# Kernel optimization log

Measured on AMD Instinct MI355X. Metric: run time of the kernel, lower is better.

The kernel has to match this reference:

```python
import jax, jax.numpy as jnp
import numpy as np
from math import factorial

# (mul, l, parity) in mul_ir layout order
IRREPS_IN1 = [(128, 0, 1), (128, 1, -1), (128, 2, 1)]
IRREPS_IN2 = [(1, 0, 1), (1, 1, -1), (1, 2, 1)]
IRREPS_OUT = [(128, 0, 1), (128, 1, -1), (128, 2, 1)]
BATCH = 65536


def _f(n):
    return float(factorial(int(round(n))))


def _su2_cg(j1, j2, j3, m1, m2, m3):
    # <j1 m1 j2 m2 | j3 m3> (Racah formula, complex SU(2) basis)
    if m3 != m1 + m2:
        return 0.0
    vmin = int(max(-j1 + j2 + m3, -j1 + m1, 0))
    vmax = int(min(j2 + j3 + m1, j3 - j1 + j2, j3 + m3))
    C = ((2 * j3 + 1) * _f(j3 + j1 - j2) * _f(j3 - j1 + j2) * _f(j1 + j2 - j3)
         * _f(j3 + m3) * _f(j3 - m3)
         / (_f(j1 + j2 + j3 + 1) * _f(j1 - m1) * _f(j1 + m1) * _f(j2 - m2) * _f(j2 + m2))) ** 0.5
    S = 0.0
    for v in range(vmin, vmax + 1):
        S += (-1.0) ** (v + j2 + m2) * _f(j2 + j3 + m1 - v) * _f(j1 - m1 + v) / (
            _f(v) * _f(j3 - j1 + j2 - v) * _f(j3 + m3 - v) * _f(v + j1 - j2 - m3))
    return C * S


def _q(l):
    # change of basis real -> complex spherical harmonics (e3nn convention)
    q = np.zeros((2 * l + 1, 2 * l + 1), dtype=np.complex128)
    for m in range(-l, 0):
        q[l + m, l + abs(m)] = 1 / np.sqrt(2)
        q[l + m, l - abs(m)] = -1j / np.sqrt(2)
    q[l, l] = 1.0
    for m in range(1, l + 1):
        q[l + m, l + abs(m)] = (-1) ** m / np.sqrt(2)
        q[l + m, l - abs(m)] = 1j * (-1) ** m / np.sqrt(2)
    return (-1j) ** l * q


def _wigner_3j(l1, l2, l3):
    C = np.zeros((2 * l1 + 1, 2 * l2 + 1, 2 * l3 + 1))
    for m1 in range(-l1, l1 + 1):
        for m2 in range(-l2, l2 + 1):
            for m3 in range(-l3, l3 + 1):
                C[l1 + m1, l2 + m2, l3 + m3] = _su2_cg(l1, l2, l3, m1, m2, m3)
    Q1, Q2, Q3 = _q(l1), _q(l2), _q(l3)
    R = np.einsum('ij,kl,nm,ikn->jlm', Q1, Q2, np.conj(Q3), C.astype(np.complex128))
    return np.real(R) / np.sqrt(2 * l3 + 1)  # sum of squares == 1 (3j normalization)


def _slices(irreps):
    out, off = [], 0
    for mul, l, _ in irreps:
        out.append((off, mul, 2 * l + 1))
        off += mul * (2 * l + 1)
    return out, off


S1, DIM1 = _slices(IRREPS_IN1)
S2, DIM2 = _slices(IRREPS_IN2)
S3, DIM3 = _slices(IRREPS_OUT)

# fully-connected instruction list: all parity/triangle-allowed (i1, i2, i3) paths
_instr = [(i1, i2, i3)
          for i1, (_, l1, p1) in enumerate(IRREPS_IN1)
          for i2, (_, l2, p2) in enumerate(IRREPS_IN2)
          for i3, (_, l3, p3) in enumerate(IRREPS_OUT)
          if p1 * p2 == p3 and abs(l1 - l2) <= l3 <= l1 + l2]

# path normalization 'element': fan-in per output irrep = sum of mul1*mul2 over incoming paths
_fan = {}
for i1, i2, i3 in _instr:
    _fan[i3] = _fan.get(i3, 0) + IRREPS_IN1[i1][0] * IRREPS_IN2[i2][0]

PATHS, _off = [], 0
for i1, i2, i3 in _instr:
    mu1, l1, _ = IRREPS_IN1[i1]
    mu2, l2, _ = IRREPS_IN2[i2]
    mu3, l3, _ = IRREPS_OUT[i3]
    # irrep_normalization 'component' + path 'element': path_weight = sqrt((2l3+1)/fan)
    cg = _wigner_3j(l1, l2, l3) * np.sqrt((2 * l3 + 1) / _fan[i3])
    PATHS.append((i1, i2, i3, _off, (mu1, mu2, mu3), jnp.asarray(cg, dtype=jnp.float32)))
    _off += mu1 * mu2 * mu3
WEIGHT_NUMEL = _off  # 180224 for these irreps (11 paths x 128*1*128)


def _fctp(x1, x2, weight):
    w = weight.reshape(-1).astype(x1.dtype)
    acc = [None] * len(IRREPS_OUT)
    for i1, i2, i3, off, wshape, cg in PATHS:
        o1, mu1, d1 = S1[i1]
        o2, mu2, d2 = S2[i2]
        a = x1[:, o1:o1 + mu1 * d1].reshape(-1, mu1, d1)  # [B, u, i]
        b = x2[:, o2:o2 + mu2 * d2].reshape(-1, mu2, d2)  # [B, v, j]
        wp = w[off:off + wshape[0] * wshape[1] * wshape[2]].reshape(wshape)  # [u, v, w]
        c = jnp.einsum('bui,bvj,uvw,ijk->bwk', a, b, wp, cg.astype(x1.dtype))
        acc[i3] = c if acc[i3] is None else acc[i3] + c
    # mul_ir layout: flatten each (B, mul, 2l+1) segment and concatenate
    return jnp.concatenate([s.reshape(s.shape[0], -1) for s in acc], axis=-1)


def setup_inputs():
    key = jax.random.key(0)
    k1, k2, k3 = jax.random.split(key, 3)
    return {
        "x1": jax.random.normal(k1, (BATCH, DIM1), dtype=jnp.float32),
        "x2": jax.random.normal(k2, (BATCH, DIM2), dtype=jnp.float32),
        "weight": jax.random.normal(k3, (1, WEIGHT_NUMEL), dtype=jnp.float32),
    }


def reference(x1, x2, weight):
    return _fctp(x1, x2, weight)
```

## Files before the change

### kernel.cpp

```cpp
#include <hip/hip_runtime.h>
#include <hip/hip_bf16.h>

typedef __attribute__((ext_vector_type(8))) short bf16x8;
typedef __attribute__((ext_vector_type(4))) float f32x4;
typedef __attribute__((ext_vector_type(4))) unsigned int u32x4;
typedef __attribute__((ext_vector_type(4))) unsigned short u16x4;

__device__ __forceinline__ unsigned short f2bf(float f) {
  __hip_bfloat16 h = __float2bfloat16(f);
  return __builtin_bit_cast(unsigned short, h);
}
__device__ __forceinline__ float bfw(unsigned int word, int hi) {
  union { unsigned int i; float f; } v;
  v.i = hi ? (word & 0xffff0000u) : (word << 16);
  return v.f;
}

struct cplx { double re, im; };
__device__ __forceinline__ cplx cmul(cplx a, cplx b) {
  return {a.re * b.re - a.im * b.im, a.re * b.im + a.im * b.re};
}
__device__ __forceinline__ double fct_(int n) {
  const double f[8] = {1., 1., 2., 6., 24., 120., 720., 5040.};
  return f[n];
}
__device__ __forceinline__ int imax_(int a, int b) { return a > b ? a : b; }
__device__ __forceinline__ int imin_(int a, int b) { return a < b ? a : b; }

__device__ double su2_cg(int j1, int j2, int j3, int m1, int m2, int m3) {
  if (m3 != m1 + m2) return 0.0;
  int vmin = imax_(imax_(-j1 + j2 + m3, -j1 + m1), 0);
  int vmax = imin_(imin_(j2 + j3 + m1, j3 - j1 + j2), j3 + m3);
  double C = sqrt((2.0 * j3 + 1.0) * fct_(j3 + j1 - j2) * fct_(j3 - j1 + j2) * fct_(j1 + j2 - j3)
                  * fct_(j3 + m3) * fct_(j3 - m3)
                  / (fct_(j1 + j2 + j3 + 1) * fct_(j1 - m1) * fct_(j1 + m1) * fct_(j2 - m2) * fct_(j2 + m2)));
  double S = 0.0;
  for (int v = vmin; v <= vmax; ++v) {
    double sgn = ((v + j2 + m2) & 1) ? -1.0 : 1.0;
    S += sgn * fct_(j2 + j3 + m1 - v) * fct_(j1 - m1 + v)
         / (fct_(v) * fct_(j3 - j1 + j2 - v) * fct_(j3 + m3 - v) * fct_(v + j1 - j2 - m3));
  }
  return C * S;
}

__device__ cplx q_entry(int l, int r, int c) {
  const double s2 = 0.70710678118654752440;
  int m = r - l;
  cplx v = {0.0, 0.0};
  if (m < 0) {
    if (c == l - m) v = {s2, 0.0};
    else if (c == l + m) v = {0.0, -s2};
  } else if (m == 0) {
    if (c == l) v = {1.0, 0.0};
  } else {
    double sgn = (m & 1) ? -1.0 : 1.0;
    if (c == l + m) v = {sgn * s2, 0.0};
    else if (c == l - m) v = {0.0, sgn * s2};
  }
  cplx f;
  switch (l & 3) {
    case 0: f = {1.0, 0.0}; break;
    case 1: f = {0.0, -1.0}; break;
    case 2: f = {-1.0, 0.0}; break;
    default: f = {0.0, 1.0}; break;
  }
  return cmul(f, v);
}

__global__ void init_kernel(const float* __restrict__ w, unsigned short* __restrict__ Wt,
                            float* __restrict__ cgw) {
  const int blk = blockIdx.x;
  const int tid = threadIdx.x;
  if (blk < 704) {
    int g = blk * 256 + tid;
    int p = g >> 14, rem = g & 16383;
    int u = rem >> 7, wc = rem & 127;
    Wt[(p << 14) + (wc << 7) + u] = f2bf(w[g]);
    return;
  }
  const int p = blk - 704;
  const int L1t[11] = {0,0,0,1,1,1,1,2,2,2,2};
  const int L2t[11] = {0,1,2,0,1,1,2,0,1,2,2};
  const int L3t[11] = {0,1,2,1,0,2,1,2,1,0,2};
  const double FAN[11] = {384.,512.,512.,512.,384.,512.,512.,512.,512.,384.,512.};
  const int l1 = L1t[p], l2 = L2t[p], l3 = L3t[p];
  const int n1 = 2 * l1 + 1, n2 = 2 * l2 + 1, n3 = 2 * l3 + 1;
  if (tid >= n1 * n2 * n3) return;
  const int a = tid / (n2 * n3), b = (tid / n3) % n2, c = tid % n3;
  double sre = 0.0;
  for (int i = 0; i < n1; ++i)
    for (int k = 0; k < n2; ++k)
      for (int n = 0; n < n3; ++n) {
        double cg = su2_cg(l1, l2, l3, i - l1, k - l2, n - l3);
        if (cg == 0.0) continue;
        cplx q1 = q_entry(l1, i, a);
        cplx q2 = q_entry(l2, k, b);
        cplx q3 = q_entry(l3, n, c);
        q3.im = -q3.im;
        cplx pr = cmul(cmul(q1, q2), q3);
        sre += pr.re * cg;
      }
  cgw[p * 125 + a * 25 + b * 5 + c] = (float)(sre / sqrt(FAN[p]));
}

__device__ __forceinline__ void stage_all(const float* __restrict__ x1, int Mbase,
                                          unsigned short* __restrict__ s_a) {
  const int tid = threadIdx.x;
#pragma unroll 6
  for (int rep = 0; rep < 18; ++rep) {
    int it = tid + rep * 256;
    int row = it / 288, c4 = it % 288;
    int col = c4 << 2;
    const f32x4 v = __builtin_nontemporal_load(
        (const f32x4*)&x1[(size_t)(Mbase + row) * 1152 + col]);
    u16x4 h;
    h.x = f2bf(v.x); h.y = f2bf(v.y); h.z = f2bf(v.z); h.w = f2bf(v.w);
    int dst;
    if (col < 128)      dst = row * 136 + col;
    else if (col < 512) dst = 2176 + row * 392 + (col - 128);
    else                dst = 8448 + row * 648 + (col - 512);
    *(u16x4*)&s_a[dst] = h;
  }
}

template<int PID, int L1, int L2, int L3>
__device__ __forceinline__ void do_path(const float* __restrict__ cgw,
                                        const unsigned short* __restrict__ s_a,
                                        const unsigned short* __restrict__ Wt,
                                        const float (&x2v)[9],
                                        int kg, int r16, int nbase,
                                        f32x4 (&acc)[2 * L3 + 1][2]) {
  constexpr int D1 = 2 * L1 + 1, D2 = 2 * L2 + 1, D3 = 2 * L3 + 1;
  constexpr int O2 = (L2 == 0) ? 0 : ((L2 == 1) ? 1 : 4);
  constexpr int GB = (L1 == 0) ? 0 : ((L1 == 1) ? 2176 : 8448);
  constexpr int pitch = 128 * D1 + 8;
  float g[D1][D3];
#pragma unroll
  for (int i = 0; i < D1; ++i)
#pragma unroll
    for (int k = 0; k < D3; ++k) {
      float s = 0.f;
#pragma unroll
      for (int j = 0; j < D2; ++j)
        s += x2v[O2 + j] * cgw[PID * 125 + i * 25 + j * 5 + k];
      g[i][k] = s;
    }
  const unsigned short* __restrict__ wbase = Wt + (PID << 14);
  const unsigned short* __restrict__ ap0 = s_a + GB + r16 * pitch;
#pragma unroll 1
  for (int us = 0; us < 4; ++us) {
    const int u0 = us * 32 + kg * 8;
    const unsigned short* ap = ap0 + u0 * D1;
    u32x4 av[D1];
#pragma unroll
    for (int d = 0; d < D1; ++d) av[d] = *(const u32x4*)(ap + d * 8);
    u32x4 bw[2];
#pragma unroll
    for (int nf = 0; nf < 2; ++nf)
      bw[nf] = *(const u32x4*)&wbase[(nbase + nf * 16 + r16) * 128 + u0];
    unsigned int taw[D3][4];
#pragma unroll
    for (int jp = 0; jp < 4; ++jp) {
      float a0[D1], a1[D1];
#pragma unroll
      for (int i = 0; i < D1; ++i) {
        int e0 = (2 * jp) * D1 + i, e1 = e0 + D1;
        a0[i] = bfw(av[e0 >> 3][(e0 & 7) >> 1], e0 & 1);
        a1[i] = bfw(av[e1 >> 3][(e1 & 7) >> 1], e1 & 1);
      }
#pragma unroll
      for (int k = 0; k < D3; ++k) {
        float t0 = 0.f, t1 = 0.f;
#pragma unroll
        for (int i = 0; i < D1; ++i) { t0 += a0[i] * g[i][k]; t1 += a1[i] * g[i][k]; }
        taw[k][jp] = (unsigned int)f2bf(t0) | ((unsigned int)f2bf(t1) << 16);
      }
    }
#pragma unroll
    for (int k = 0; k < D3; ++k) {
      u32x4 tw;
      tw.x = taw[k][0]; tw.y = taw[k][1]; tw.z = taw[k][2]; tw.w = taw[k][3];
      bf16x8 ta = __builtin_bit_cast(bf16x8, tw);
#pragma unroll
      for (int nf = 0; nf < 2; ++nf)
        acc[k][nf] = __builtin_amdgcn_mfma_f32_16x16x32_bf16(
            ta, __builtin_bit_cast(bf16x8, bw[nf]), acc[k][nf], 0, 0, 0);
    }
  }
}

__global__ void __launch_bounds__(256, 2) fctp_main(
    const float* __restrict__ x1, const float* __restrict__ x2,
    const float* __restrict__ cgw, const unsigned short* __restrict__ Wt,
    float* __restrict__ out) {
  __shared__ __align__(16) unsigned short s_a[18816];
  const int tid = threadIdx.x;
  const int Mbase = blockIdx.x << 4;

  stage_all(x1, Mbase, s_a);

  const int lane = tid & 63, ni = tid >> 6;
  const int r16 = lane & 15, kg = lane >> 4;
  const int nbase = ni << 5;

  float x2v[9];
  const float* __restrict__ x2p = x2 + (size_t)(Mbase + r16) * 9;
#pragma unroll
  for (int j = 0; j < 9; ++j) x2v[j] = x2p[j];

  __syncthreads();

  const int bout = Mbase + (kg << 2);

  {
    f32x4 acc[1][2] = {};
    do_path<0, 0, 0, 0>(cgw, s_a, Wt, x2v, kg, r16, nbase, acc);
    do_path<4, 1, 1, 0>(cgw, s_a, Wt, x2v, kg, r16, nbase, acc);
    do_path<9, 2, 2, 0>(cgw, s_a, Wt, x2v, kg, r16, nbase, acc);
#pragma unroll
    for (int nf = 0; nf < 2; ++nf) {
      const int w = nbase + nf * 16 + r16;
#pragma unroll
      for (int r = 0; r < 4; ++r)
        __builtin_nontemporal_store(acc[0][nf][r],
                                    &out[(size_t)(bout + r) * 1152 + w]);
    }
  }
  {
    f32x4 acc[3][2] = {};
    do_path<1, 0, 1, 1>(cgw, s_a, Wt, x2v, kg, r16, nbase, acc);
    do_path<3, 1, 0, 1>(cgw, s_a, Wt, x2v, kg, r16, nbase, acc);
    do_path<6, 1, 2, 1>(cgw, s_a, Wt, x2v, kg, r16, nbase, acc);
    do_path<8, 2, 1, 1>(cgw, s_a, Wt, x2v, kg, r16, nbase, acc);
#pragma unroll
    for (int nf = 0; nf < 2; ++nf) {
      const int w = nbase + nf * 16 + r16;
#pragma unroll
      for (int r = 0; r < 4; ++r) {
        float* o = out + (size_t)(bout + r) * 1152 + 128 + w * 3;
#pragma unroll
        for (int k = 0; k < 3; ++k) o[k] = acc[k][nf][r];
      }
    }
  }
  {
    f32x4 acc[5][2] = {};
    do_path<2, 0, 2, 2>(cgw, s_a, Wt, x2v, kg, r16, nbase, acc);
    do_path<5, 1, 1, 2>(cgw, s_a, Wt, x2v, kg, r16, nbase, acc);
    do_path<7, 2, 0, 2>(cgw, s_a, Wt, x2v, kg, r16, nbase, acc);
    do_path<10, 2, 2, 2>(cgw, s_a, Wt, x2v, kg, r16, nbase, acc);
#pragma unroll
    for (int nf = 0; nf < 2; ++nf) {
      const int w = nbase + nf * 16 + r16;
#pragma unroll
      for (int r = 0; r < 4; ++r) {
        float* o = out + (size_t)(bout + r) * 1152 + 512 + w * 5;
#pragma unroll
        for (int k = 0; k < 5; ++k) o[k] = acc[k][nf][r];
      }
    }
  }
}

extern "C" void kernel_launch(void* const* d_in, const int* in_sizes, int n_in,
                              void* d_out, int out_size, void* d_ws, size_t ws_size,
                              hipStream_t stream) {
  (void)in_sizes; (void)n_in; (void)out_size; (void)ws_size;
  const float* x1 = (const float*)d_in[0];
  const float* x2 = (const float*)d_in[1];
  const float* w  = (const float*)d_in[2];
  float* out = (float*)d_out;
  float* cgw = (float*)d_ws;
  unsigned short* Wt = (unsigned short*)((char*)d_ws + 8192);
  init_kernel<<<dim3(715), dim3(256), 0, stream>>>(w, Wt, cgw);
  fctp_main<<<dim3(4096), dim3(256), 0, stream>>>(x1, x2, cgw, Wt, out);
}
```

Baseline: 283.0 us.

## Reassociate contraction: MFMA x1 with weights first, apply CG-x2 coefficients after

Reorders the tensor-product contraction so each input component of x1 is multiplied by the weight matrix on MFMA first, then combined with precomputed per-row CG·x2 coefficients stored in LDS. This removes per-slice VALU contractions and bf16 repacking of the intermediate, keeping it in fp32. It restages x1 into a component-major LDS layout using scalar stores and adds a small gmap table built in the init kernel. Register pressure rises from the per-component accumulators.

Result: slower. 485.7 us (+71.6%).

```diff
diff --git a/kernel.cpp b/kernel.cpp
--- a/kernel.cpp
+++ b/kernel.cpp
@@ -4,16 +4,10 @@
 typedef __attribute__((ext_vector_type(8))) short bf16x8;
 typedef __attribute__((ext_vector_type(4))) float f32x4;
 typedef __attribute__((ext_vector_type(4))) unsigned int u32x4;
-typedef __attribute__((ext_vector_type(4))) unsigned short u16x4;
 
 __device__ __forceinline__ unsigned short f2bf(float f) {
   __hip_bfloat16 h = __float2bfloat16(f);
   return __builtin_bit_cast(unsigned short, h);
-}
-__device__ __forceinline__ float bfw(unsigned int word, int hi) {
-  union { unsigned int i; float f; } v;
-  v.i = hi ? (word & 0xffff0000u) : (word << 16);
-  return v.f;
 }
 
 struct cplx { double re, im; };
@@ -68,7 +62,7 @@
 }
 
 __global__ void init_kernel(const float* __restrict__ w, unsigned short* __restrict__ Wt,
-                            float* __restrict__ cgw) {
+                            float* __restrict__ cgw, unsigned int* __restrict__ gmap) {
   const int blk = blockIdx.x;
   const int tid = threadIdx.x;
   if (blk < 704) {
@@ -76,6 +70,20 @@
     int p = g >> 14, rem = g & 16383;
     int u = rem >> 7, wc = rem & 127;
     Wt[(p << 14) + (wc << 7) + u] = f2bf(w[g]);
+    return;
+  }
+  if (blk == 715) {
+    if (tid < 115) {
+      const int PBt[12] = {0,1,4,9,18,21,36,45,70,85,90,115};
+      const int D2t[11] = {1,3,5,1,3,3,5,1,3,5,5};
+      const int D3t[11] = {1,3,5,3,1,5,3,5,3,1,5};
+      const int O2t[11] = {0,1,4,0,1,1,4,0,1,4,4};
+      int p = 0;
+      while (tid >= PBt[p + 1]) ++p;
+      int le = tid - PBt[p];
+      int i = le / D3t[p], k = le % D3t[p];
+      gmap[tid] = ((unsigned)(p * 125 + i * 25 + k) << 8) | (O2t[p] << 4) | D2t[p];
+    }
     return;
   }
   const int p = blk - 704;
@@ -106,117 +114,114 @@
 __device__ __forceinline__ void stage_all(const float* __restrict__ x1, int Mbase,
                                           unsigned short* __restrict__ s_a) {
   const int tid = threadIdx.x;
-#pragma unroll 6
+#pragma unroll 4
   for (int rep = 0; rep < 18; ++rep) {
     int it = tid + rep * 256;
     int row = it / 288, c4 = it % 288;
     int col = c4 << 2;
     const f32x4 v = __builtin_nontemporal_load(
         (const f32x4*)&x1[(size_t)(Mbase + row) * 1152 + col]);
-    u16x4 h;
-    h.x = f2bf(v.x); h.y = f2bf(v.y); h.z = f2bf(v.z); h.w = f2bf(v.w);
-    int dst;
-    if (col < 128)      dst = row * 136 + col;
-    else if (col < 512) dst = 2176 + row * 392 + (col - 128);
-    else                dst = 8448 + row * 648 + (col - 512);
-    *(u16x4*)&s_a[dst] = h;
-  }
-}
-
-template<int PID, int L1, int L2, int L3>
-__device__ __forceinline__ void do_path(const float* __restrict__ cgw,
-                                        const unsigned short* __restrict__ s_a,
+    unsigned short* sr = s_a + row * 132;
+    if (col < 128) {
+#pragma unroll
+      for (int q = 0; q < 4; ++q) sr[col + q] = f2bf(v[q]);
+    } else if (col < 512) {
+      int cc = col - 128;
+#pragma unroll
+      for (int q = 0; q < 4; ++q) {
+        int u = (cc + q) / 3, i = (cc + q) % 3;
+        sr[(1 + i) * 2112 + u] = f2bf(v[q]);
+      }
+    } else {
+      int cc = col - 512;
+#pragma unroll
+      for (int q = 0; q < 4; ++q) {
+        int u = (cc + q) / 5, i = (cc + q) % 5;
+        sr[(4 + i) * 2112 + u] = f2bf(v[q]);
+      }
+    }
+  }
+}
+
+template<int PID, int L1, int L3, int PBASE>
+__device__ __forceinline__ void do_path(const unsigned short* __restrict__ s_a,
+                                        const float* __restrict__ g_lds,
                                         const unsigned short* __restrict__ Wt,
-                                        const float (&x2v)[9],
                                         int kg, int r16, int nbase,
                                         f32x4 (&acc)[2 * L3 + 1][2]) {
-  constexpr int D1 = 2 * L1 + 1, D2 = 2 * L2 + 1, D3 = 2 * L3 + 1;
-  constexpr int O2 = (L2 == 0) ? 0 : ((L2 == 1) ? 1 : 4);
-  constexpr int GB = (L1 == 0) ? 0 : ((L1 == 1) ? 2176 : 8448);
-  constexpr int pitch = 128 * D1 + 8;
-  float g[D1][D3];
+  constexpr int D1 = 2 * L1 + 1, D3 = 2 * L3 + 1;
+  constexpr int GB = (L1 == 0) ? 0 : ((L1 == 1) ? 2112 : 8448);
+  f32x4 y[D1][2];
 #pragma unroll
   for (int i = 0; i < D1; ++i)
 #pragma unroll
-    for (int k = 0; k < D3; ++k) {
-      float s = 0.f;
-#pragma unroll
-      for (int j = 0; j < D2; ++j)
-        s += x2v[O2 + j] * cgw[PID * 125 + i * 25 + j * 5 + k];
-      g[i][k] = s;
-    }
+    for (int nf = 0; nf < 2; ++nf) y[i][nf] = f32x4{0.f, 0.f, 0.f, 0.f};
   const unsigned short* __restrict__ wbase = Wt + (PID << 14);
-  const unsigned short* __restrict__ ap0 = s_a + GB + r16 * pitch;
 #pragma unroll 1
   for (int us = 0; us < 4; ++us) {
     const int u0 = us * 32 + kg * 8;
-    const unsigned short* ap = ap0 + u0 * D1;
-    u32x4 av[D1];
-#pragma unroll
-    for (int d = 0; d < D1; ++d) av[d] = *(const u32x4*)(ap + d * 8);
+    const unsigned short* ap = s_a + GB + r16 * 132 + u0;
+    u32x4 af[D1];
+#pragma unroll
+    for (int d = 0; d < D1; ++d) af[d] = *(const u32x4*)(ap + d * 2112);
     u32x4 bw[2];
 #pragma unroll
     for (int nf = 0; nf < 2; ++nf)
       bw[nf] = *(const u32x4*)&wbase[(nbase + nf * 16 + r16) * 128 + u0];
-    unsigned int taw[D3][4];
-#pragma unroll
-    for (int jp = 0; jp < 4; ++jp) {
-      float a0[D1], a1[D1];
-#pragma unroll
-      for (int i = 0; i < D1; ++i) {
-        int e0 = (2 * jp) * D1 + i, e1 = e0 + D1;
-        a0[i] = bfw(av[e0 >> 3][(e0 & 7) >> 1], e0 & 1);
-        a1[i] = bfw(av[e1 >> 3][(e1 & 7) >> 1], e1 & 1);
-      }
-#pragma unroll
-      for (int k = 0; k < D3; ++k) {
-        float t0 = 0.f, t1 = 0.f;
-#pragma unroll
-        for (int i = 0; i < D1; ++i) { t0 += a0[i] * g[i][k]; t1 += a1[i] * g[i][k]; }
-        taw[k][jp] = (unsigned int)f2bf(t0) | ((unsigned int)f2bf(t1) << 16);
-      }
-    }
+#pragma unroll
+    for (int i = 0; i < D1; ++i)
+#pragma unroll
+      for (int nf = 0; nf < 2; ++nf)
+        y[i][nf] = __builtin_amdgcn_mfma_f32_16x16x32_bf16(
+            __builtin_bit_cast(bf16x8, af[i]), __builtin_bit_cast(bf16x8, bw[nf]),
+            y[i][nf], 0, 0, 0);
+  }
+#pragma unroll
+  for (int i = 0; i < D1; ++i)
 #pragma unroll
     for (int k = 0; k < D3; ++k) {
-      u32x4 tw;
-      tw.x = taw[k][0]; tw.y = taw[k][1]; tw.z = taw[k][2]; tw.w = taw[k][3];
-      bf16x8 ta = __builtin_bit_cast(bf16x8, tw);
-#pragma unroll
-      for (int nf = 0; nf < 2; ++nf)
-        acc[k][nf] = __builtin_amdgcn_mfma_f32_16x16x32_bf16(
-            ta, __builtin_bit_cast(bf16x8, bw[nf]), acc[k][nf], 0, 0, 0);
-    }
-  }
+      const f32x4 g4 = *(const f32x4*)&g_lds[((PBASE + i * D3 + k) << 4) + (kg << 2)];
+#pragma unroll
+      for (int nf = 0; nf < 2; ++nf) acc[k][nf] += g4 * y[i][nf];
+    }
 }
 
 __global__ void __launch_bounds__(256, 2) fctp_main(
     const float* __restrict__ x1, const float* __restrict__ x2,
-    const float* __restrict__ cgw, const unsigned short* __restrict__ Wt,
-    float* __restrict__ out) {
-  __shared__ __align__(16) unsigned short s_a[18816];
+    const float* __restrict__ cgw, const unsigned int* __restrict__ gmap,
+    const unsigned short* __restrict__ Wt, float* __restrict__ out) {
+  __shared__ __align__(16) unsigned short s_a[19008];
+  __shared__ __align__(16) float g_lds[1840];
   const int tid = threadIdx.x;
   const int Mbase = blockIdx.x << 4;
 
   stage_all(x1, Mbase, s_a);
+
+#pragma unroll 1
+  for (int t = tid; t < 1840; t += 256) {
+    int row = t & 15, e = t >> 4;
+    unsigned m = gmap[e];
+    int d2 = m & 15, o2 = (m >> 4) & 15, co = m >> 8;
+    const float* xp = x2 + (size_t)(Mbase + row) * 9 + o2;
+    const float* cp = cgw + co;
+    float s = 0.f;
+    for (int j = 0; j < d2; ++j) s += xp[j] * cp[j * 5];
+    g_lds[(e << 4) + row] = s;
+  }
 
   const int lane = tid & 63, ni = tid >> 6;
   const int r16 = lane & 15, kg = lane >> 4;
   const int nbase = ni << 5;
 
-  float x2v[9];
-  const float* __restrict__ x2p = x2 + (size_t)(Mbase + r16) * 9;
-#pragma unroll
-  for (int j = 0; j < 9; ++j) x2v[j] = x2p[j];
-
   __syncthreads();
 
   const int bout = Mbase + (kg << 2);
 
   {
     f32x4 acc[1][2] = {};
-    do_path<0, 0, 0, 0>(cgw, s_a, Wt, x2v, kg, r16, nbase, acc);
-    do_path<4, 1, 1, 0>(cgw, s_a, Wt, x2v, kg, r16, nbase, acc);
-    do_path<9, 2, 2, 0>(cgw, s_a, Wt, x2v, kg, r16, nbase, acc);
+    do_path<0, 0, 0, 0>(s_a, g_lds, Wt, kg, r16, nbase, acc);
+    do_path<4, 1, 0, 18>(s_a, g_lds, Wt, kg, r16, nbase, acc);
+    do_path<9, 2, 0, 85>(s_a, g_lds, Wt, kg, r16, nbase, acc);
 #pragma unroll
     for (int nf = 0; nf < 2; ++nf) {
       const int w = nbase + nf * 16 + r16;
@@ -228,10 +233,10 @@
   }
   {
     f32x4 acc[3][2] = {};
-    do_path<1, 0, 1, 1>(cgw, s_a, Wt, x2v, kg, r16, nbase, acc);
-    do_path<3, 1, 0, 1>(cgw, s_a, Wt, x2v, kg, r16, nbase, acc);
-    do_path<6, 1, 2, 1>(cgw, s_a, Wt, x2v, kg, r16, nbase, acc);
-    do_path<8, 2, 1, 1>(cgw, s_a, Wt, x2v, kg, r16, nbase, acc);
+    do_path<1, 0, 1, 1>(s_a, g_lds, Wt, kg, r16, nbase, acc);
+    do_path<3, 1, 1, 9>(s_a, g_lds, Wt, kg, r16, nbase, acc);
+    do_path<6, 1, 1, 36>(s_a, g_lds, Wt, kg, r16, nbase, acc);
+    do_path<8, 2, 1, 70>(s_a, g_lds, Wt, kg, r16, nbase, acc);
 #pragma unroll
     for (int nf = 0; nf < 2; ++nf) {
       const int w = nbase + nf * 16 + r16;
@@ -245,10 +250,10 @@
   }
   {
     f32x4 acc[5][2] = {};
-    do_path<2, 0, 2, 2>(cgw, s_a, Wt, x2v, kg, r16, nbase, acc);
-    do_path<5, 1, 1, 2>(cgw, s_a, Wt, x2v, kg, r16, nbase, acc);
-    do_path<7, 2, 0, 2>(cgw, s_a, Wt, x2v, kg, r16, nbase, acc);
-    do_path<10, 2, 2, 2>(cgw, s_a, Wt, x2v, kg, r16, nbase, acc);
+    do_path<2, 0, 2, 4>(s_a, g_lds, Wt, kg, r16, nbase, acc);
+    do_path<5, 1, 2, 21>(s_a, g_lds, Wt, kg, r16, nbase, acc);
+    do_path<7, 2, 2, 45>(s_a, g_lds, Wt, kg, r16, nbase, acc);
+    do_path<10, 2, 2, 90>(s_a, g_lds, Wt, kg, r16, nbase, acc);
 #pragma unroll
     for (int nf = 0; nf < 2; ++nf) {
       const int w = nbase + nf * 16 + r16;
@@ -271,7 +276,8 @@
   const float* w  = (const float*)d_in[2];
   float* out = (float*)d_out;
   float* cgw = (float*)d_ws;
+  unsigned int* gmap = (unsigned int*)((char*)d_ws + 5504);
   unsigned short* Wt = (unsigned short*)((char*)d_ws + 8192);
-  init_kernel<<<dim3(715), dim3(256), 0, stream>>>(w, Wt, cgw);
-  fctp_main<<<dim3(4096), dim3(256), 0, stream>>>(x1, x2, cgw, Wt, out);
-}
+  init_kernel<<<dim3(716), dim3(256), 0, stream>>>(w, Wt, cgw, gmap);
+  fctp_main<<<dim3(4096), dim3(256), 0, stream>>>(x1, x2, cgw, gmap, Wt, out);
+}
```
